# Performance work log

Measured on AMD Instinct MI355X. Metric: run time of the kernel, lower is better.

The kernel has to match this reference:

```python
import jax, jax.numpy as jnp
import numpy as np

EPS = 1e-12  # torch F.normalize eps

def _l2norm(v, axis):
    n = jnp.sqrt(jnp.sum(v * v, axis=axis, keepdims=True))
    return v / jnp.maximum(n, EPS)

def setup_inputs() -> dict:
    key = jax.random.key(0)
    k1, k2, k3 = jax.random.split(key, 3)
    B, D, H, W, K = 64, 512, 30, 40, 64
    x = jax.random.normal(k1, (B, D, H, W), dtype=jnp.float32)
    conv_w = jax.random.normal(k2, (K, D), dtype=jnp.float32)  # 1x1 conv weight, no bias (vladv1)
    centroids = jax.random.uniform(k3, (K, D), dtype=jnp.float32)
    return {"x": x, "conv_w": conv_w, "centroids": centroids}

def reference(x, conv_w, centroids):
    B, D, H, W = x.shape
    K = centroids.shape[0]
    # L2-normalize input descriptors over channel dim
    x = _l2norm(x, axis=1)
    xf = x.reshape(B, D, H * W)                       # (B, D, N)
    # 1x1 conv == per-pixel matmul; softmax over clusters
    logits = jnp.einsum('bdn,kd->bkn', xf, conv_w)    # (B, K, N)
    a = jax.nn.softmax(logits, axis=1)                # (B, K, N)
    # VLAD residual aggregation, loop-free:
    # vlad[b,k,d] = sum_n a[b,k,n] * (x[b,d,n] - c[k,d])
    vlad = jnp.einsum('bkn,bdn->bkd', a, xf) - a.sum(axis=-1)[..., None] * centroids[None]
    # intra-normalize per cluster, flatten, global L2 norm
    vlad = _l2norm(vlad, axis=2)
    v = vlad.reshape(B, K * D)
    return _l2norm(v, axis=1)
```

## Files before the change

kernel.cpp:

```cpp
#include <hip/hip_runtime.h>

#define B_ 64
#define D_ 512
#define N_ 1200
#define K_ 64
#define NT2CNT 19
#define AST 1216
#define NSTEP 38
#define NT3 16
#define PT 32
#define NTILES 38

typedef __attribute__((ext_vector_type(8))) short bf16x8;
typedef __attribute__((ext_vector_type(4))) float f32x4;

__device__ __forceinline__ float bf2f(unsigned short u) {
  union { unsigned int i; float f; } v; v.i = ((unsigned int)u) << 16; return v.f;
}
__device__ __forceinline__ unsigned short f2bf(float f) {
  unsigned int u = __float_as_uint(f);
  u += 0x7FFFu + ((u >> 16) & 1u);
  return (unsigned short)(u >> 16);
}

__global__ __launch_bounds__(64) void k_wsplit(
    const float* __restrict__ w,
    unsigned short* __restrict__ wfh, unsigned short* __restrict__ wfl)
{
  const int blk = blockIdx.x;
  const int wv = blk >> 4, dstep = blk & 15;
  const int l = threadIdx.x;
  const int row = wv * 16 + (l & 15);
  const int dbase = dstep * 32 + 8 * (l >> 4);
  const size_t o = ((size_t)blk * 64 + l) * 8;
#pragma unroll
  for (int j = 0; j < 8; ++j) {
    const float v = w[row * D_ + dbase + j];
    const unsigned int u = __float_as_uint(v);
    const unsigned int h = u & 0xFFFF0000u;
    wfh[o + j] = (unsigned short)(h >> 16);
    wfl[o + j] = f2bf(v - __uint_as_float(h));
  }
}

__global__ __launch_bounds__(256) void k_logits_mfma(
    const float* __restrict__ x, const unsigned short* __restrict__ wfh,
    const unsigned short* __restrict__ wfl, unsigned short* __restrict__ a_bf,
    float* __restrict__ invn_ws, float* __restrict__ asum_part, int folded)
{
  const int nt = blockIdx.x, b = blockIdx.y;
  const int n0 = nt * 64;
  const int t = threadIdx.x;
  const int lane = t & 63, wv = t >> 6;

  __shared__ __align__(16) unsigned short xbuf[2][2][64][136];
  __shared__ float nsq_s[4][64];
  __shared__ float red_s[3][64];
  float (*ls)[66] = reinterpret_cast<float(*)[66]>(&xbuf[0][0][0][0]);

  const int n_l = t & 63, dg = t >> 6;
  const int nc = min(n0 + n_l, N_ - 1);
  const float* xb = x + (size_t)b * D_ * N_ + nc;
  float nsq = 0.f;

  f32x4 acc[4] = {{0.f,0.f,0.f,0.f},{0.f,0.f,0.f,0.f},{0.f,0.f,0.f,0.f},{0.f,0.f,0.f,0.f}};

  auto conv = [&](int c, int buf) {
    const int db = c * 128 + dg * 32;
#pragma unroll
    for (int i = 0; i < 32; i += 4) {
      const float f0 = xb[(size_t)(db + i + 0) * N_];
      const float f1 = xb[(size_t)(db + i + 1) * N_];
      const float f2 = xb[(size_t)(db + i + 2) * N_];
      const float f3 = xb[(size_t)(db + i + 3) * N_];
      nsq += f0 * f0 + f1 * f1 + f2 * f2 + f3 * f3;
      const unsigned int u0 = __float_as_uint(f0), u1 = __float_as_uint(f1);
      const unsigned int u2 = __float_as_uint(f2), u3 = __float_as_uint(f3);
      const unsigned int h0 = u0 & 0xFFFF0000u, h1 = u1 & 0xFFFF0000u;
      const unsigned int h2 = u2 & 0xFFFF0000u, h3 = u3 & 0xFFFF0000u;
      ushort4 hv, lv;
      hv.x = (unsigned short)(h0 >> 16); hv.y = (unsigned short)(h1 >> 16);
      hv.z = (unsigned short)(h2 >> 16); hv.w = (unsigned short)(h3 >> 16);
      lv.x = f2bf(f0 - __uint_as_float(h0)); lv.y = f2bf(f1 - __uint_as_float(h1));
      lv.z = f2bf(f2 - __uint_as_float(h2)); lv.w = f2bf(f3 - __uint_as_float(h3));
      *(ushort4*)&xbuf[buf][0][n_l][dg * 32 + i] = hv;
      *(ushort4*)&xbuf[buf][1][n_l][dg * 32 + i] = lv;
    }
  };

  auto mstep = [&](int c, int buf) {
#pragma unroll
    for (int ds = 0; ds < 4; ++ds) {
      const int fi = (wv * 16 + c * 4 + ds) * 64 + lane;
      const bf16x8 ah = ((const bf16x8*)wfh)[fi];
      const bf16x8 al = ((const bf16x8*)wfl)[fi];
#pragma unroll
      for (int s = 0; s < 4; ++s) {
        const unsigned short* ph = &xbuf[buf][0][s * 16 + (lane & 15)][ds * 32 + 8 * (lane >> 4)];
        const unsigned short* pl = &xbuf[buf][1][s * 16 + (lane & 15)][ds * 32 + 8 * (lane >> 4)];
        const bf16x8 bh = *(const bf16x8*)ph;
        const bf16x8 bl = *(const bf16x8*)pl;
        acc[s] = __builtin_amdgcn_mfma_f32_16x16x32_bf16(ah, bh, acc[s], 0, 0, 0);
        acc[s] = __builtin_amdgcn_mfma_f32_16x16x32_bf16(al, bh, acc[s], 0, 0, 0);
        acc[s] = __builtin_amdgcn_mfma_f32_16x16x32_bf16(ah, bl, acc[s], 0, 0, 0);
      }
    }
  };

  conv(0, 0);
  __syncthreads();
  for (int c = 0; c < 4; ++c) {
    if (c < 3) conv(c + 1, (c + 1) & 1);
    mstep(c, c & 1);
    __syncthreads();
  }

  nsq_s[dg][n_l] = nsq;
  __syncthreads();
  if (t < 64) {
    const float s4 = nsq_s[0][t] + nsq_s[1][t] + nsq_s[2][t] + nsq_s[3][t];
    const float inv = 1.f / fmaxf(sqrtf(s4), 1e-12f);
    red_s[0][t] = inv;
    if (n0 + t < N_) invn_ws[b * N_ + n0 + t] = inv;
  }
  __syncthreads();

#pragma unroll
  for (int s = 0; s < 4; ++s) {
    const int n = 16 * s + (lane & 15);
    const float inv = red_s[0][n];
#pragma unroll
    for (int r = 0; r < 4; ++r) {
      const int k = 16 * wv + 4 * (lane >> 4) + r;
      ls[k][n] = acc[s][r] * inv;
    }
  }
  __syncthreads();

  if (t < 64) {
    float m = -1e30f;
    for (int k = 0; k < K_; ++k) m = fmaxf(m, ls[k][t]);
    float ssum = 0.f;
    for (int k = 0; k < K_; ++k) ssum += __expf(ls[k][t] - m);
    red_s[1][t] = m;
    red_s[2][t] = 1.f / ssum;
  }
  __syncthreads();

#pragma unroll
  for (int s = 0; s < 4; ++s) {
    const int n = 16 * s + (lane & 15);
    const bool valid = (n0 + n) < N_;
    const float inv = red_s[0][n], mv = red_s[1][n], si = red_s[2][n];
#pragma unroll
    for (int r = 0; r < 4; ++r) {
      const int k = 16 * wv + 4 * (lane >> 4) + r;
      const float av = valid ? __expf(acc[s][r] * inv - mv) * si : 0.f;
      ls[k][n] = av;
      if (folded) {
        a_bf[((size_t)b * K_ + k) * AST + n0 + n] = f2bf(av * inv);
      } else if (valid) {
        a_bf[((size_t)b * K_ + k) * N_ + n0 + n] = f2bf(av);
      }
    }
  }
  __syncthreads();

  if (t < K_) {
    float su = 0.f;
#pragma unroll 8
    for (int p = 0; p < 64; ++p) su += ls[t][p];
    asum_part[(b * NT2CNT + nt) * K_ + t] = su;
  }
}

__global__ __launch_bounds__(256) void k_vlad_mfma(
    const float* __restrict__ x, const unsigned short* __restrict__ a_bf,
    float* __restrict__ vlad_ws)
{
  const int id = blockIdx.x;
  const int b  = id >> 2;
  const int dc = id & 3;
  const int t = threadIdx.x;
  const int lane = t & 63, wv = t >> 6;

  __shared__ __align__(16) unsigned short xs[2][2][128][40];

  f32x4 acc[8];
#pragma unroll
  for (int i = 0; i < 8; ++i) acc[i] = (f32x4){0.f, 0.f, 0.f, 0.f};

  const int sr = t >> 1, sh = t & 1;
  const float* xrow = x + (size_t)b * D_ * N_ + (size_t)(dc * 128 + sr) * N_;

  auto stage = [&](int s, int buf) {
    const int nb = s * 32 + sh * 16;
#pragma unroll
    for (int i = 0; i < 4; ++i) {
      const int nn = nb + 4 * i;
      float4 v = make_float4(0.f, 0.f, 0.f, 0.f);
      if (nn < N_) v = *(const float4*)(xrow + nn);
      const unsigned int u0 = __float_as_uint(v.x), u1 = __float_as_uint(v.y);
      const unsigned int u2 = __float_as_uint(v.z), u3 = __float_as_uint(v.w);
      const unsigned int h0 = u0 & 0xFFFF0000u, h1 = u1 & 0xFFFF0000u;
      const unsigned int h2 = u2 & 0xFFFF0000u, h3 = u3 & 0xFFFF0000u;
      ushort4 hv, lv;
      hv.x = (unsigned short)(h0 >> 16); hv.y = (unsigned short)(h1 >> 16);
      hv.z = (unsigned short)(h2 >> 16); hv.w = (unsigned short)(h3 >> 16);
      lv.x = f2bf(v.x - __uint_as_float(h0)); lv.y = f2bf(v.y - __uint_as_float(h1));
      lv.z = f2bf(v.z - __uint_as_float(h2)); lv.w = f2bf(v.w - __uint_as_float(h3));
      *(ushort4*)&xs[buf][0][sr][sh * 16 + 4 * i] = hv;
      *(ushort4*)&xs[buf][1][sr][sh * 16 + 4 * i] = lv;
    }
  };

  const unsigned short* arow =
      a_bf + ((size_t)b * K_ + 16 * wv + (lane & 15)) * AST + 8 * (lane >> 4);

  auto compute = [&](int s, int buf) {
    const bf16x8 af = *(const bf16x8*)(arow + s * 32);
#pragma unroll
    for (int st = 0; st < 8; ++st) {
      const unsigned short* ph = &xs[buf][0][st * 16 + (lane & 15)][8 * (lane >> 4)];
      const unsigned short* pl = &xs[buf][1][st * 16 + (lane & 15)][8 * (lane >> 4)];
      const bf16x8 bh = *(const bf16x8*)ph;
      const bf16x8 bl = *(const bf16x8*)pl;
      acc[st] = __builtin_amdgcn_mfma_f32_16x16x32_bf16(af, bh, acc[st], 0, 0, 0);
      acc[st] = __builtin_amdgcn_mfma_f32_16x16x32_bf16(af, bl, acc[st], 0, 0, 0);
    }
  };

  stage(0, 0);
  __syncthreads();
  for (int s = 0; s < NSTEP; ++s) {
    if (s < NSTEP - 1) stage(s + 1, (s + 1) & 1);
    compute(s, s & 1);
    __syncthreads();
  }

  const size_t kb = (size_t)b * K_ + 16 * wv + 4 * (lane >> 4);
  const int db = dc * 128 + (lane & 15);
#pragma unroll
  for (int st = 0; st < 8; ++st)
#pragma unroll
    for (int r = 0; r < 4; ++r)
      vlad_ws[(kb + r) * D_ + db + st * 16] = acc[st][r];
}

__global__ __launch_bounds__(256) void k_norm(
    const float* __restrict__ vlad_ws, const float* __restrict__ asum_part,
    const float* __restrict__ cent, float* __restrict__ out)
{
  const int id = blockIdx.x;
  const int kg = id >> 6;
  const int b  = id & 63;
  const int t  = threadIdx.x;
  __shared__ float asums[8];
  __shared__ float part[8][4];
  __shared__ float scale_s[8];

  if (t < 8) {
    float s = 0.f;
    for (int nt2 = 0; nt2 < NT2CNT; ++nt2)
      s += asum_part[(b * NT2CNT + nt2) * K_ + kg * 8 + t];
    asums[t] = s;
  }
  __syncthreads();

  const int d0 = 2 * t;
  const int lane = t & 63, wv = t >> 6;
  float acc[16];
#pragma unroll
  for (int j = 0; j < 8; ++j) {
    const int k = kg * 8 + j;
    const float2 v  = *(const float2*)(vlad_ws + ((size_t)b * K_ + k) * D_ + d0);
    const float2 c2 = *(const float2*)(cent + (size_t)k * D_ + d0);
    const float asv = asums[j];
    acc[j * 2]     = v.x - asv * c2.x;
    acc[j * 2 + 1] = v.y - asv * c2.y;
    float s = acc[j * 2] * acc[j * 2] + acc[j * 2 + 1] * acc[j * 2 + 1];
#pragma unroll
    for (int o = 32; o > 0; o >>= 1) s += __shfl_down(s, o, 64);
    if (lane == 0) part[j][wv] = s;
  }
  __syncthreads();
  if (t < 8) {
    const float s = part[t][0] + part[t][1] + part[t][2] + part[t][3];
    scale_s[t] = 0.125f / fmaxf(sqrtf(s), 1e-12f);
  }
  __syncthreads();
#pragma unroll
  for (int j = 0; j < 8; ++j) {
    const int k = kg * 8 + j;
    const float f = scale_s[j];
    float2 o;
    o.x = acc[j * 2] * f;
    o.y = acc[j * 2 + 1] * f;
    *(float2*)(out + ((size_t)b * K_ + k) * D_ + d0) = o;
  }
}

__global__ __launch_bounds__(256) void k_vlad(
    const float* __restrict__ x, const unsigned short* __restrict__ a_bf,
    const float* __restrict__ invn_ws, const float* __restrict__ asum_part,
    const float* __restrict__ cent, float* __restrict__ out)
{
  const int id = blockIdx.x;
  const int kg = id >> 6;
  const int b  = id & 63;
  const int t  = threadIdx.x;
  __shared__ float xs[NT3][518];
  __shared__ float as[8][NT3 + 2];
  __shared__ float asums[8];
  __shared__ float part[8][4];
  __shared__ float scale_s[8];

  if (t < 8) {
    float s = 0.f;
    for (int nt2 = 0; nt2 < NT2CNT; ++nt2)
      s += asum_part[(b * NT2CNT + nt2) * K_ + kg * 8 + t];
    asums[t] = s;
  }
  float acc[16];
#pragma unroll
  for (int i = 0; i < 16; ++i) acc[i] = 0.f;

  const float* xb = x + (size_t)b * D_ * N_;
  const int d0 = 2 * t;
  const int snl = t & 15, sdc = t >> 4;
  const int saj = t >> 4, sanl = t & 15;

  for (int n0 = 0; n0 < N_; n0 += NT3) {
    __syncthreads();
    {
      const float* xp = xb + (size_t)(sdc * 32) * N_ + (n0 + snl);
      float* xrow = &xs[snl][sdc * 32];
#pragma unroll
      for (int i = 0; i < 32; i += 2) {
        float2 w2;
        w2.x = xp[(size_t)i * N_];
        w2.y = xp[(size_t)(i + 1) * N_];
        *(float2*)(xrow + i) = w2;
      }
    }
    if (t < 128) {
      const float av = bf2f(a_bf[((size_t)b * K_ + kg * 8 + saj) * N_ + n0 + sanl])
                     * invn_ws[b * N_ + n0 + sanl];
      as[saj][sanl] = av;
    }
    __syncthreads();
#pragma unroll 2
    for (int nl = 0; nl < NT3; nl += 2) {
      const float2 x0 = *(const float2*)(&xs[nl][d0]);
      const float2 x1 = *(const float2*)(&xs[nl + 1][d0]);
#pragma unroll
      for (int j = 0; j < 8; ++j) {
        const float2 a2 = *(const float2*)(&as[j][nl]);
        acc[j * 2]     = fmaf(a2.x, x0.x, fmaf(a2.y, x1.x, acc[j * 2]));
        acc[j * 2 + 1] = fmaf(a2.x, x0.y, fmaf(a2.y, x1.y, acc[j * 2 + 1]));
      }
    }
  }
  __syncthreads();
  const int lane = t & 63, wv = t >> 6;
#pragma unroll
  for (int j = 0; j < 8; ++j) {
    const int k = kg * 8 + j;
    const float asv = asums[j];
    const float2 c2 = *(const float2*)(cent + (size_t)k * D_ + d0);
    acc[j * 2]     -= asv * c2.x;
    acc[j * 2 + 1] -= asv * c2.y;
    float v = acc[j * 2] * acc[j * 2] + acc[j * 2 + 1] * acc[j * 2 + 1];
#pragma unroll
    for (int o = 32; o > 0; o >>= 1) v += __shfl_down(v, o, 64);
    if (lane == 0) part[j][wv] = v;
  }
  __syncthreads();
  if (t < 8) {
    const float s = part[t][0] + part[t][1] + part[t][2] + part[t][3];
    scale_s[t] = 0.125f / fmaxf(sqrtf(s), 1e-12f);
  }
  __syncthreads();
#pragma unroll
  for (int j = 0; j < 8; ++j) {
    const int k = kg * 8 + j;
    const float f = scale_s[j];
    float2 o;
    o.x = acc[j * 2] * f;
    o.y = acc[j * 2 + 1] * f;
    *(float2*)(out + ((size_t)b * K_ + k) * D_ + d0) = o;
  }
}

__global__ __launch_bounds__(256) void k_logits(
    const float* __restrict__ x, const float* __restrict__ w,
    unsigned short* __restrict__ a_bf, float* __restrict__ invn_ws,
    float* __restrict__ asum_part)
{
  const int nt = blockIdx.x, b = blockIdx.y;
  const int t = threadIdx.x;
  const int px = t & 63;
  const int kg = t >> 6;
  const int n = nt * 64 + px;
  const bool valid = (n < N_);
  const int nc = valid ? n : (N_ - 1);
  __shared__ float lsh[K_][65];

  const float* xb = x + (size_t)b * D_ * N_ + nc;
  const float* wg = w + kg * 16 * D_;

  float acc[16];
#pragma unroll
  for (int j = 0; j < 16; ++j) acc[j] = 0.f;
  float nsq = 0.f;

  for (int d = 0; d < D_; d += 4) {
    const float xv0 = xb[(size_t)(d + 0) * N_];
    const float xv1 = xb[(size_t)(d + 1) * N_];
    const float xv2 = xb[(size_t)(d + 2) * N_];
    const float xv3 = xb[(size_t)(d + 3) * N_];
    nsq += xv0 * xv0 + xv1 * xv1 + xv2 * xv2 + xv3 * xv3;
#pragma unroll
    for (int j = 0; j < 16; ++j) {
      const float4 wv = *(const float4*)(wg + j * D_ + d);
      acc[j] = fmaf(xv0, wv.x, fmaf(xv1, wv.y, fmaf(xv2, wv.z, fmaf(xv3, wv.w, acc[j]))));
    }
  }
  const float invn = 1.f / fmaxf(sqrtf(nsq), 1e-12f);
  if (kg == 0 && valid) invn_ws[b * N_ + n] = invn;
#pragma unroll
  for (int j = 0; j < 16; ++j) lsh[kg * 16 + j][px] = acc[j] * invn;
  __syncthreads();
  float m = -1e30f;
  for (int k = 0; k < K_; ++k) m = fmaxf(m, lsh[k][px]);
  float s = 0.f;
  for (int k = 0; k < K_; ++k) s += __expf(lsh[k][px] - m);
  const float sinv = 1.f / s;
  float av[16];
#pragma unroll
  for (int j = 0; j < 16; ++j)
    av[j] = valid ? __expf(acc[j] * invn - m) * sinv : 0.f;
  __syncthreads();
#pragma unroll
  for (int j = 0; j < 16; ++j) lsh[kg * 16 + j][px] = av[j];
  if (valid) {
#pragma unroll
    for (int j = 0; j < 16; ++j)
      a_bf[((size_t)b * K_ + kg * 16 + j) * N_ + n] = f2bf(av[j]);
  }
  __syncthreads();
  if (t < K_) {
    float su = 0.f;
#pragma unroll 8
    for (int p = 0; p < 64; ++p) su += lsh[t][p];
    asum_part[(b * NT2CNT + nt) * K_ + t] = su;
  }
}

__global__ __launch_bounds__(256) void k_fused(
    const float* __restrict__ x, const float* __restrict__ w,
    const float* __restrict__ cent, float* __restrict__ out)
{
  const int id = blockIdx.x;
  const int kq = id >> 6;
  const int b  = id & 63;
  const int t  = threadIdx.x;
  const int px = t & 31;
  const int kg = t >> 5;
  const bool own = (kg >> 1) == kq;
  const int khbase = (kg & 1) * 8;

  __shared__ unsigned short xs[PT][514];
  __shared__ float ls[K_][33];
  __shared__ float a_s[16][34];
  __shared__ float araw[16][34];
  __shared__ float asums[16];
  __shared__ float part[16][4];
  __shared__ float scale_s[16];

  if (t < 16) asums[t] = 0.f;
  float acc[32];
#pragma unroll
  for (int i = 0; i < 32; ++i) acc[i] = 0.f;
  const float* xb = x + (size_t)b * D_ * N_;

  for (int tile = 0; tile < NTILES; ++tile) {
    const int n0 = tile * PT;
    {
      const int row = t & 31, chunk = t >> 5;
      const int n = n0 + row;
      const int nc = (n < N_) ? n : (N_ - 1);
      const float* xp = xb + (size_t)(chunk * 64) * N_ + nc;
#pragma unroll
      for (int i = 0; i < 64; ++i)
        xs[row][chunk * 64 + i] = f2bf(xp[(size_t)i * N_]);
    }
    __syncthreads();
    float invn;
    {
      const ushort2* xr = (const ushort2*)xs[px];
      float lg[8] = {0,0,0,0,0,0,0,0};
      float nsq = 0.f;
      const float* wbase = w + (size_t)(kg * 8) * D_;
      for (int du = 0; du < D_ / 4; ++du) {
        const ushort2 p0 = xr[2 * du], p1 = xr[2 * du + 1];
        const float x0 = bf2f(p0.x), x1 = bf2f(p0.y), x2 = bf2f(p1.x), x3 = bf2f(p1.y);
        nsq += x0 * x0 + x1 * x1 + x2 * x2 + x3 * x3;
#pragma unroll
        for (int j = 0; j < 8; ++j) {
          const float4 wv = *(const float4*)(wbase + j * D_ + 4 * du);
          lg[j] = fmaf(x0,wv.x,fmaf(x1,wv.y,fmaf(x2,wv.z,fmaf(x3,wv.w,lg[j]))));
        }
      }
      invn = 1.f / fmaxf(sqrtf(nsq), 1e-12f);
#pragma unroll
      for (int j = 0; j < 8; ++j) ls[kg * 8 + j][px] = lg[j] * invn;
    }
    __syncthreads();
    {
      const bool valid = (n0 + px) < N_;
      float m = -1e30f;
      for (int k = 0; k < K_; ++k) m = fmaxf(m, ls[k][px]);
      float s = 0.f;
      for (int k = 0; k < K_; ++k) s += __expf(ls[k][px] - m);
      const float sinv = 1.f / s;
      if (own) {
#pragma unroll
        for (int j = 0; j < 8; ++j) {
          const float av = valid ? __expf(ls[kg * 8 + j][px] - m) * sinv : 0.f;
          araw[khbase + j][px] = av;
          a_s[khbase + j][px]  = av * invn;
        }
      }
    }
    __syncthreads();
    if (t < 16) {
      float su = 0.f;
#pragma unroll 8
      for (int p = 0; p < PT; ++p) su += araw[t][p];
      asums[t] += su;
    }
    {
#pragma unroll 2
      for (int nl = 0; nl < PT; nl += 2) {
        const ushort2 u0 = ((const ushort2*)xs[nl])[t];
        const ushort2 u1 = ((const ushort2*)xs[nl + 1])[t];
        const float x00 = bf2f(u0.x), x01 = bf2f(u0.y);
        const float x10 = bf2f(u1.x), x11 = bf2f(u1.y);
#pragma unroll
        for (int kh = 0; kh < 16; ++kh) {
          const float2 a2 = *(const float2*)(&a_s[kh][nl]);
          acc[kh * 2]     = fmaf(a2.x, x00, fmaf(a2.y, x10, acc[kh * 2]));
          acc[kh * 2 + 1] = fmaf(a2.x, x01, fmaf(a2.y, x11, acc[kh * 2 + 1]));
        }
      }
    }
    __syncthreads();
  }
  const int d0 = 2 * t;
  const int lane = t & 63, wv = t >> 6;
#pragma unroll
  for (int kh = 0; kh < 16; ++kh) {
    const int k = kq * 16 + kh;
    const float asv = asums[kh];
    const float2 c2 = *(const float2*)(cent + (size_t)k * D_ + d0);
    acc[kh * 2]     -= asv * c2.x;
    acc[kh * 2 + 1] -= asv * c2.y;
    float v = acc[kh * 2] * acc[kh * 2] + acc[kh * 2 + 1] * acc[kh * 2 + 1];
#pragma unroll
    for (int o = 32; o > 0; o >>= 1) v += __shfl_down(v, o, 64);
    if (lane == 0) part[kh][wv] = v;
  }
  __syncthreads();
  if (t < 16) {
    const float s = part[t][0] + part[t][1] + part[t][2] + part[t][3];
    scale_s[t] = 0.125f / fmaxf(sqrtf(s), 1e-12f);
  }
  __syncthreads();
#pragma unroll
  for (int kh = 0; kh < 16; ++kh) {
    const int k = kq * 16 + kh;
    const float f = scale_s[kh];
    float2 o;
    o.x = acc[kh * 2] * f;
    o.y = acc[kh * 2 + 1] * f;
    *(float2*)(out + ((size_t)b * K_ + k) * D_ + d0) = o;
  }
}

extern "C" void kernel_launch(void* const* d_in, const int* in_sizes, int n_in,
                              void* d_out, int out_size, void* d_ws, size_t ws_size,
                              hipStream_t stream)
{
  const float* x  = (const float*)d_in[0];
  const float* w  = (const float*)d_in[1];
  const float* ct = (const float*)d_in[2];
  float* out = (float*)d_out;

  const size_t wf_u16  = (size_t)K_ * D_;
  const size_t invn_f  = (size_t)B_ * N_;
  const size_t asum_f  = (size_t)B_ * NT2CNT * K_;
  const size_t a_u16   = (size_t)B_ * K_ * N_;
  const size_t ap_u16  = (size_t)B_ * K_ * AST;
  const size_t vlad_f  = (size_t)B_ * K_ * D_;
  const size_t need_old  = (invn_f + asum_f) * 4 + a_u16 * 2;
  const size_t need_mfma = need_old + wf_u16 * 2 * 2;
  const size_t need_v2   = wf_u16 * 2 * 2 + ap_u16 * 2
                         + (invn_f + asum_f + vlad_f) * 4;

  if (ws_size >= need_v2) {
    unsigned short* wfh = (unsigned short*)d_ws;
    unsigned short* wfl = wfh + wf_u16;
    unsigned short* a_bf = wfl + wf_u16;
    float* invn_ws   = (float*)(a_bf + ap_u16);
    float* asum_part = invn_ws + invn_f;
    float* vlad_ws   = asum_part + asum_f;
    hipLaunchKernelGGL(k_wsplit, dim3(64), dim3(64), 0, stream, w, wfh, wfl);
    hipLaunchKernelGGL(k_logits_mfma, dim3(NT2CNT, B_), dim3(256), 0, stream,
                       x, wfh, wfl, a_bf, invn_ws, asum_part, 1);
    hipLaunchKernelGGL(k_vlad_mfma, dim3(256), dim3(256), 0, stream,
                       x, a_bf, vlad_ws);
    hipLaunchKernelGGL(k_norm, dim3(512), dim3(256), 0, stream,
                       vlad_ws, asum_part, ct, out);
  } else if (ws_size >= need_mfma) {
    unsigned short* wfh = (unsigned short*)d_ws;
    unsigned short* wfl = wfh + wf_u16;
    float* invn_ws   = (float*)(wfl + wf_u16);
    float* asum_part = invn_ws + invn_f;
    unsigned short* a_bf = (unsigned short*)(asum_part + asum_f);
    hipLaunchKernelGGL(k_wsplit, dim3(64), dim3(64), 0, stream, w, wfh, wfl);
    hipLaunchKernelGGL(k_logits_mfma, dim3(NT2CNT, B_), dim3(256), 0, stream,
                       x, wfh, wfl, a_bf, invn_ws, asum_part, 0);
    hipLaunchKernelGGL(k_vlad, dim3(512), dim3(256), 0, stream,
                       x, a_bf, invn_ws, asum_part, ct, out);
  } else if (ws_size >= need_old) {
    float* invn_ws   = (float*)d_ws;
    float* asum_part = invn_ws + invn_f;
    unsigned short* a_bf = (unsigned short*)(asum_part + asum_f);
    hipLaunchKernelGGL(k_logits, dim3(NT2CNT, B_), dim3(256), 0, stream,
                       x, w, a_bf, invn_ws, asum_part);
    hipLaunchKernelGGL(k_vlad, dim3(512), dim3(256), 0, stream,
                       x, a_bf, invn_ws, asum_part, ct, out);
  } else {
    hipLaunchKernelGGL(k_fused, dim3(256), dim3(256), 0, stream, x, w, ct, out);
  }
}
```

Baseline: 312.6 us.

## Swizzle LDS fragment layout, split vlad N-range, and overlap global loads with MFMA

Both MFMA kernels now write the x operand into shared memory in fragment-major order, so each lane reads its bf16x8 operand contiguously, which is meant to cut LDS bank conflicts and address arithmetic. The logits kernel loads the next chunk into registers before the MFMA step and converts it afterwards, hiding global latency behind compute. The vlad kernel splits the pixel range in two, doubling the grid to 512 blocks for occupancy, and writes two partial buffers that the norm kernel sums. Both kernels get launch_bounds occupancy hints, at the cost of more register pressure, a second vlad workspace and extra read traffic in the norm kernel.

Result: faster. 287.2 us (-8.1%).

```diff
diff --git a/kernel.cpp b/kernel.cpp
--- a/kernel.cpp
+++ b/kernel.cpp
@@ -6,46 +6,47 @@
 #define K_ 64
 #define NT2CNT 19
 #define AST 1216
-#define NSTEP 38
 #define NT3 16
 #define PT 32
 #define NTILES 38
 
+typedef unsigned short u16;
 typedef __attribute__((ext_vector_type(8))) short bf16x8;
+typedef __attribute__((ext_vector_type(8))) unsigned short u16x8;
 typedef __attribute__((ext_vector_type(4))) float f32x4;
 
-__device__ __forceinline__ float bf2f(unsigned short u) {
+__device__ __forceinline__ float bf2f(u16 u) {
   union { unsigned int i; float f; } v; v.i = ((unsigned int)u) << 16; return v.f;
 }
-__device__ __forceinline__ unsigned short f2bf(float f) {
+__device__ __forceinline__ u16 f2bf(float f) {
   unsigned int u = __float_as_uint(f);
   u += 0x7FFFu + ((u >> 16) & 1u);
-  return (unsigned short)(u >> 16);
+  return (u16)(u >> 16);
 }
 
 __global__ __launch_bounds__(64) void k_wsplit(
     const float* __restrict__ w,
-    unsigned short* __restrict__ wfh, unsigned short* __restrict__ wfl)
+    u16* __restrict__ wfh, u16* __restrict__ wfl)
 {
   const int blk = blockIdx.x;
-  const int wv = blk >> 4, dstep = blk & 15;
+  const int wv = blk >> 4, kk = blk & 15;
   const int l = threadIdx.x;
   const int row = wv * 16 + (l & 15);
-  const int dbase = dstep * 32 + 8 * (l >> 4);
+  const int dbase = kk * 32 + 8 * (l >> 4);
   const size_t o = ((size_t)blk * 64 + l) * 8;
 #pragma unroll
   for (int j = 0; j < 8; ++j) {
     const float v = w[row * D_ + dbase + j];
     const unsigned int u = __float_as_uint(v);
     const unsigned int h = u & 0xFFFF0000u;
-    wfh[o + j] = (unsigned short)(h >> 16);
+    wfh[o + j] = (u16)(h >> 16);
     wfl[o + j] = f2bf(v - __uint_as_float(h));
   }
 }
 
-__global__ __launch_bounds__(256) void k_logits_mfma(
-    const float* __restrict__ x, const unsigned short* __restrict__ wfh,
-    const unsigned short* __restrict__ wfl, unsigned short* __restrict__ a_bf,
+__global__ __launch_bounds__(256, 4) void k_logits_mfma(
+    const float* __restrict__ x, const u16* __restrict__ wfh,
+    const u16* __restrict__ wfl, u16* __restrict__ a_bf,
     float* __restrict__ invn_ws, float* __restrict__ asum_part, int folded)
 {
   const int nt = blockIdx.x, b = blockIdx.y;
@@ -53,7 +54,7 @@
   const int t = threadIdx.x;
   const int lane = t & 63, wv = t >> 6;
 
-  __shared__ __align__(16) unsigned short xbuf[2][2][64][136];
+  __shared__ __align__(16) u16 xbuf[2][2][512][8];
   __shared__ float nsq_s[4][64];
   __shared__ float red_s[3][64];
   float (*ls)[66] = reinterpret_cast<float(*)[66]>(&xbuf[0][0][0][0]);
@@ -65,41 +66,42 @@
 
   f32x4 acc[4] = {{0.f,0.f,0.f,0.f},{0.f,0.f,0.f,0.f},{0.f,0.f,0.f,0.f},{0.f,0.f,0.f,0.f}};
 
-  auto conv = [&](int c, int buf) {
-    const int db = c * 128 + dg * 32;
-#pragma unroll
-    for (int i = 0; i < 32; i += 4) {
-      const float f0 = xb[(size_t)(db + i + 0) * N_];
-      const float f1 = xb[(size_t)(db + i + 1) * N_];
-      const float f2 = xb[(size_t)(db + i + 2) * N_];
-      const float f3 = xb[(size_t)(db + i + 3) * N_];
-      nsq += f0 * f0 + f1 * f1 + f2 * f2 + f3 * f3;
-      const unsigned int u0 = __float_as_uint(f0), u1 = __float_as_uint(f1);
-      const unsigned int u2 = __float_as_uint(f2), u3 = __float_as_uint(f3);
-      const unsigned int h0 = u0 & 0xFFFF0000u, h1 = u1 & 0xFFFF0000u;
-      const unsigned int h2 = u2 & 0xFFFF0000u, h3 = u3 & 0xFFFF0000u;
-      ushort4 hv, lv;
-      hv.x = (unsigned short)(h0 >> 16); hv.y = (unsigned short)(h1 >> 16);
-      hv.z = (unsigned short)(h2 >> 16); hv.w = (unsigned short)(h3 >> 16);
-      lv.x = f2bf(f0 - __uint_as_float(h0)); lv.y = f2bf(f1 - __uint_as_float(h1));
-      lv.z = f2bf(f2 - __uint_as_float(h2)); lv.w = f2bf(f3 - __uint_as_float(h3));
-      *(ushort4*)&xbuf[buf][0][n_l][dg * 32 + i] = hv;
-      *(ushort4*)&xbuf[buf][1][n_l][dg * 32 + i] = lv;
-    }
+  const int kkl_w = dg >> 1;
+  const int qb    = (dg & 1) * 2;
+  const int slotw = kkl_w * 256 + (n_l >> 4) * 64 + qb * 16 + (n_l & 15);
+
+  auto loadf = [&](int c, float* f) {
+    const int db = c * 64 + dg * 16;
+#pragma unroll
+    for (int e = 0; e < 16; ++e) f[e] = xb[(size_t)(db + e) * N_];
   };
-
+  auto cvtwrite = [&](const float* f, int buf) {
+    u16x8 h0{}, h1{}, l0{}, l1{};
+#pragma unroll
+    for (int e = 0; e < 16; ++e) {
+      nsq += f[e] * f[e];
+      const unsigned int u = __float_as_uint(f[e]);
+      const unsigned int hi = u & 0xFFFF0000u;
+      const u16 hh = (u16)(hi >> 16);
+      const u16 ll = f2bf(f[e] - __uint_as_float(hi));
+      if (e < 8) { h0[e] = (short)hh; l0[e] = (short)ll; }
+      else       { h1[e - 8] = (short)hh; l1[e - 8] = (short)ll; }
+    }
+    *(u16x8*)xbuf[buf][0][slotw]      = h0;
+    *(u16x8*)xbuf[buf][0][slotw + 16] = h1;
+    *(u16x8*)xbuf[buf][1][slotw]      = l0;
+    *(u16x8*)xbuf[buf][1][slotw + 16] = l1;
+  };
   auto mstep = [&](int c, int buf) {
 #pragma unroll
-    for (int ds = 0; ds < 4; ++ds) {
-      const int fi = (wv * 16 + c * 4 + ds) * 64 + lane;
+    for (int kkl = 0; kkl < 2; ++kkl) {
+      const int fi = (wv * 16 + c * 2 + kkl) * 64 + lane;
       const bf16x8 ah = ((const bf16x8*)wfh)[fi];
       const bf16x8 al = ((const bf16x8*)wfl)[fi];
 #pragma unroll
       for (int s = 0; s < 4; ++s) {
-        const unsigned short* ph = &xbuf[buf][0][s * 16 + (lane & 15)][ds * 32 + 8 * (lane >> 4)];
-        const unsigned short* pl = &xbuf[buf][1][s * 16 + (lane & 15)][ds * 32 + 8 * (lane >> 4)];
-        const bf16x8 bh = *(const bf16x8*)ph;
-        const bf16x8 bl = *(const bf16x8*)pl;
+        const bf16x8 bh = *(const bf16x8*)xbuf[buf][0][kkl * 256 + s * 64 + lane];
+        const bf16x8 bl = *(const bf16x8*)xbuf[buf][1][kkl * 256 + s * 64 + lane];
         acc[s] = __builtin_amdgcn_mfma_f32_16x16x32_bf16(ah, bh, acc[s], 0, 0, 0);
         acc[s] = __builtin_amdgcn_mfma_f32_16x16x32_bf16(al, bh, acc[s], 0, 0, 0);
         acc[s] = __builtin_amdgcn_mfma_f32_16x16x32_bf16(ah, bl, acc[s], 0, 0, 0);
@@ -107,11 +109,14 @@
     }
   };
 
-  conv(0, 0);
-  __syncthreads();
-  for (int c = 0; c < 4; ++c) {
-    if (c < 3) conv(c + 1, (c + 1) & 1);
+  { float f[16]; loadf(0, f); cvtwrite(f, 0); }
+  __syncthreads();
+#pragma unroll
+  for (int c = 0; c < 8; ++c) {
+    float f[16];
+    if (c < 7) loadf(c + 1, f);
     mstep(c, c & 1);
+    if (c < 7) cvtwrite(f, (c + 1) & 1);
     __syncthreads();
   }
 
@@ -121,7 +126,7 @@
     const float s4 = nsq_s[0][t] + nsq_s[1][t] + nsq_s[2][t] + nsq_s[3][t];
     const float inv = 1.f / fmaxf(sqrtf(s4), 1e-12f);
     red_s[0][t] = inv;
-    if (n0 + t < N_) invn_ws[b * N_ + n0 + t] = inv;
+    if (n0 + t < N_) invn_ws[b * N_ + t + n0] = inv;
   }
   __syncthreads();
 
@@ -174,17 +179,18 @@
   }
 }
 
-__global__ __launch_bounds__(256) void k_vlad_mfma(
-    const float* __restrict__ x, const unsigned short* __restrict__ a_bf,
+__global__ __launch_bounds__(256, 4) void k_vlad_mfma(
+    const float* __restrict__ x, const u16* __restrict__ a_bf,
     float* __restrict__ vlad_ws)
 {
   const int id = blockIdx.x;
-  const int b  = id >> 2;
-  const int dc = id & 3;
+  const int b  = id >> 3;
+  const int dc = (id >> 1) & 3;
+  const int ns = id & 1;
   const int t = threadIdx.x;
   const int lane = t & 63, wv = t >> 6;
 
-  __shared__ __align__(16) unsigned short xs[2][2][128][40];
+  __shared__ __align__(16) u16 xs[2][2][512][8];
 
   f32x4 acc[8];
 #pragma unroll
@@ -192,59 +198,71 @@
 
   const int sr = t >> 1, sh = t & 1;
   const float* xrow = x + (size_t)b * D_ * N_ + (size_t)(dc * 128 + sr) * N_;
-
-  auto stage = [&](int s, int buf) {
-    const int nb = s * 32 + sh * 16;
+  const int slotw = (sr >> 4) * 64 + (sh * 2) * 16 + (sr & 15);
+
+  auto loadf = [&](int s, float4* vr) {
+    const int nb = (ns * 19 + s) * 32 + sh * 16;
 #pragma unroll
     for (int i = 0; i < 4; ++i) {
       const int nn = nb + 4 * i;
-      float4 v = make_float4(0.f, 0.f, 0.f, 0.f);
-      if (nn < N_) v = *(const float4*)(xrow + nn);
-      const unsigned int u0 = __float_as_uint(v.x), u1 = __float_as_uint(v.y);
-      const unsigned int u2 = __float_as_uint(v.z), u3 = __float_as_uint(v.w);
-      const unsigned int h0 = u0 & 0xFFFF0000u, h1 = u1 & 0xFFFF0000u;
-      const unsigned int h2 = u2 & 0xFFFF0000u, h3 = u3 & 0xFFFF0000u;
-      ushort4 hv, lv;
-      hv.x = (unsigned short)(h0 >> 16); hv.y = (unsigned short)(h1 >> 16);
-      hv.z = (unsigned short)(h2 >> 16); hv.w = (unsigned short)(h3 >> 16);
-      lv.x = f2bf(v.x - __uint_as_float(h0)); lv.y = f2bf(v.y - __uint_as_float(h1));
-      lv.z = f2bf(v.z - __uint_as_float(h2)); lv.w = f2bf(v.w - __uint_as_float(h3));
-      *(ushort4*)&xs[buf][0][sr][sh * 16 + 4 * i] = hv;
-      *(ushort4*)&xs[buf][1][sr][sh * 16 + 4 * i] = lv;
+      vr[i] = (nn < N_) ? *(const float4*)(xrow + nn)
+                        : make_float4(0.f, 0.f, 0.f, 0.f);
     }
   };
-
-  const unsigned short* arow =
-      a_bf + ((size_t)b * K_ + 16 * wv + (lane & 15)) * AST + 8 * (lane >> 4);
+  auto cvtwrite = [&](const float4* vr, int buf) {
+    u16x8 h0{}, h1{}, l0{}, l1{};
+#pragma unroll
+    for (int i = 0; i < 4; ++i) {
+      const float fv[4] = {vr[i].x, vr[i].y, vr[i].z, vr[i].w};
+#pragma unroll
+      for (int j = 0; j < 4; ++j) {
+        const int e = 4 * i + j;
+        const unsigned int u = __float_as_uint(fv[j]);
+        const unsigned int hi = u & 0xFFFF0000u;
+        const u16 hh = (u16)(hi >> 16);
+        const u16 ll = f2bf(fv[j] - __uint_as_float(hi));
+        if (e < 8) { h0[e] = (short)hh; l0[e] = (short)ll; }
+        else       { h1[e - 8] = (short)hh; l1[e - 8] = (short)ll; }
+      }
+    }
+    *(u16x8*)xs[buf][0][slotw]      = h0;
+    *(u16x8*)xs[buf][0][slotw + 16] = h1;
+    *(u16x8*)xs[buf][1][slotw]      = l0;
+    *(u16x8*)xs[buf][1][slotw + 16] = l1;
+  };
+
+  const u16* arow = a_bf + ((size_t)b * K_ + 16 * wv + (lane & 15)) * AST + 8 * (lane >> 4);
 
   auto compute = [&](int s, int buf) {
-    const bf16x8 af = *(const bf16x8*)(arow + s * 32);
+    const bf16x8 af = *(const bf16x8*)(arow + (ns * 19 + s) * 32);
 #pragma unroll
     for (int st = 0; st < 8; ++st) {
-      const unsigned short* ph = &xs[buf][0][st * 16 + (lane & 15)][8 * (lane >> 4)];
-      const unsigned short* pl = &xs[buf][1][st * 16 + (lane & 15)][8 * (lane >> 4)];
-      const bf16x8 bh = *(const bf16x8*)ph;
-      const bf16x8 bl = *(const bf16x8*)pl;
+      const bf16x8 bh = *(const bf16x8*)xs[buf][0][st * 64 + lane];
+      const bf16x8 bl = *(const bf16x8*)xs[buf][1][st * 64 + lane];
       acc[st] = __builtin_amdgcn_mfma_f32_16x16x32_bf16(af, bh, acc[st], 0, 0, 0);
       acc[st] = __builtin_amdgcn_mfma_f32_16x16x32_bf16(af, bl, acc[st], 0, 0, 0);
     }
   };
 
-  stage(0, 0);
-  __syncthreads();
-  for (int s = 0; s < NSTEP; ++s) {
-    if (s < NSTEP - 1) stage(s + 1, (s + 1) & 1);
+  { float4 vr[4]; loadf(0, vr); cvtwrite(vr, 0); }
+  __syncthreads();
+#pragma unroll 2
+  for (int s = 0; s < 19; ++s) {
+    float4 vr[4];
+    if (s < 18) loadf(s + 1, vr);
     compute(s, s & 1);
-    __syncthreads();
-  }
-
+    if (s < 18) cvtwrite(vr, (s + 1) & 1);
+    __syncthreads();
+  }
+
+  float* vp = vlad_ws + (size_t)ns * B_ * K_ * D_;
   const size_t kb = (size_t)b * K_ + 16 * wv + 4 * (lane >> 4);
   const int db = dc * 128 + (lane & 15);
 #pragma unroll
   for (int st = 0; st < 8; ++st)
 #pragma unroll
     for (int r = 0; r < 4; ++r)
-      vlad_ws[(kb + r) * D_ + db + st * 16] = acc[st][r];
+      vp[(kb + r) * D_ + db + st * 16] = acc[st][r];
 }
 
 __global__ __launch_bounds__(256) void k_norm(
@@ -269,15 +287,18 @@
 
   const int d0 = 2 * t;
   const int lane = t & 63, wv = t >> 6;
+  const size_t vhalf = (size_t)B_ * K_ * D_;
   float acc[16];
 #pragma unroll
   for (int j = 0; j < 8; ++j) {
     const int k = kg * 8 + j;
-    const float2 v  = *(const float2*)(vlad_ws + ((size_t)b * K_ + k) * D_ + d0);
+    const size_t vofs = ((size_t)b * K_ + k) * D_ + d0;
+    const float2 v0 = *(const float2*)(vlad_ws + vofs);
+    const float2 v1 = *(const float2*)(vlad_ws + vhalf + vofs);
     const float2 c2 = *(const float2*)(cent + (size_t)k * D_ + d0);
     const float asv = asums[j];
-    acc[j * 2]     = v.x - asv * c2.x;
-    acc[j * 2 + 1] = v.y - asv * c2.y;
+    acc[j * 2]     = v0.x + v1.x - asv * c2.x;
+    acc[j * 2 + 1] = v0.y + v1.y - asv * c2.y;
     float s = acc[j * 2] * acc[j * 2] + acc[j * 2 + 1] * acc[j * 2 + 1];
 #pragma unroll
     for (int o = 32; o > 0; o >>= 1) s += __shfl_down(s, o, 64);
@@ -301,7 +322,7 @@
 }
 
 __global__ __launch_bounds__(256) void k_vlad(
-    const float* __restrict__ x, const unsigned short* __restrict__ a_bf,
+    const float* __restrict__ x, const u16* __restrict__ a_bf,
     const float* __restrict__ invn_ws, const float* __restrict__ asum_part,
     const float* __restrict__ cent, float* __restrict__ out)
 {
@@ -394,7 +415,7 @@
 
 __global__ __launch_bounds__(256) void k_logits(
     const float* __restrict__ x, const float* __restrict__ w,
-    unsigned short* __restrict__ a_bf, float* __restrict__ invn_ws,
+    u16* __restrict__ a_bf, float* __restrict__ invn_ws,
     float* __restrict__ asum_part)
 {
   const int nt = blockIdx.x, b = blockIdx.y;
@@ -470,7 +491,7 @@
   const bool own = (kg >> 1) == kq;
   const int khbase = (kg & 1) * 8;
 
-  __shared__ unsigned short xs[PT][514];
+  __shared__ u16 xs[PT][514];
   __shared__ float ls[K_][33];
   __shared__ float a_s[16][34];
   __shared__ float araw[16][34];
@@ -606,28 +627,28 @@
   const size_t need_old  = (invn_f + asum_f) * 4 + a_u16 * 2;
   const size_t need_mfma = need_old + wf_u16 * 2 * 2;
   const size_t need_v2   = wf_u16 * 2 * 2 + ap_u16 * 2
-                         + (invn_f + asum_f + vlad_f) * 4;
+                         + (invn_f + asum_f + vlad_f * 2) * 4;
 
   if (ws_size >= need_v2) {
-    unsigned short* wfh = (unsigned short*)d_ws;
-    unsigned short* wfl = wfh + wf_u16;
-    unsigned short* a_bf = wfl + wf_u16;
+    u16* wfh = (u16*)d_ws;
+    u16* wfl = wfh + wf_u16;
+    u16* a_bf = wfl + wf_u16;
     float* invn_ws   = (float*)(a_bf + ap_u16);
     float* asum_part = invn_ws + invn_f;
     float* vlad_ws   = asum_part + asum_f;
     hipLaunchKernelGGL(k_wsplit, dim3(64), dim3(64), 0, stream, w, wfh, wfl);
     hipLaunchKernelGGL(k_logits_mfma, dim3(NT2CNT, B_), dim3(256), 0, stream,
                        x, wfh, wfl, a_bf, invn_ws, asum_part, 1);
-    hipLaunchKernelGGL(k_vlad_mfma, dim3(256), dim3(256), 0, stream,
+    hipLaunchKernelGGL(k_vlad_mfma, dim3(512), dim3(256), 0, stream,
                        x, a_bf, vlad_ws);
     hipLaunchKernelGGL(k_norm, dim3(512), dim3(256), 0, stream,
                        vlad_ws, asum_part, ct, out);
   } else if (ws_size >= need_mfma) {
-    unsigned short* wfh = (unsigned short*)d_ws;
-    unsigned short* wfl = wfh + wf_u16;
+    u16* wfh = (u16*)d_ws;
+    u16* wfl = wfh + wf_u16;
     float* invn_ws   = (float*)(wfl + wf_u16);
     float* asum_part = invn_ws + invn_f;
-    unsigned short* a_bf = (unsigned short*)(asum_part + asum_f);
+    u16* a_bf = (u16*)(asum_part + asum_f);
     hipLaunchKernelGGL(k_wsplit, dim3(64), dim3(64), 0, stream, w, wfh, wfl);
     hipLaunchKernelGGL(k_logits_mfma, dim3(NT2CNT, B_), dim3(256), 0, stream,
                        x, wfh, wfl, a_bf, invn_ws, asum_part, 0);
@@ -636,7 +657,7 @@
   } else if (ws_size >= need_old) {
     float* invn_ws   = (float*)d_ws;
     float* asum_part = invn_ws + invn_f;
-    unsigned short* a_bf = (unsigned short*)(asum_part + asum_f);
+    u16* a_bf = (u16*)(asum_part + asum_f);
     hipLaunchKernelGGL(k_logits, dim3(NT2CNT, B_), dim3(256), 0, stream,
                        x, w, a_bf, invn_ws, asum_part);
     hipLaunchKernelGGL(k_vlad, dim3(512), dim3(256), 0, stream,
```
